# Performance work log

Hardware: AMD Instinct MI355X
Metric: run time of the kernel (lower is better)

## Reference

```python
import jax, jax.numpy as jnp
import numpy as np
import math

B, T, D = 4, 4096, 512
LN_EPS = 1e-5


def setup_inputs() -> dict:
    key = jax.random.key(0)
    ks = jax.random.split(key, 12)
    stdv = 1.0 / math.sqrt(D)
    lin = 1.0 / math.sqrt(D)  # torch Linear default init bound
    return {
        "query": jax.random.normal(ks[0], (B, T, D), jnp.float32),
        "value": jax.random.normal(ks[1], (B, T, D), jnp.float32),
        "query_vector": jax.random.uniform(ks[2], (D,), jnp.float32, -stdv, stdv),
        "key_vector": jax.random.uniform(ks[3], (D,), jnp.float32, -stdv, stdv),
        "value_vector": jax.random.uniform(ks[4], (D,), jnp.float32, -stdv, stdv),
        "Wq": jax.random.uniform(ks[5], (D, D), jnp.float32, -lin, lin),
        "bq": jax.random.uniform(ks[6], (D,), jnp.float32, -lin, lin),
        "ln_gamma": jnp.ones((D,), jnp.float32),
        "ln_beta": jnp.zeros((D,), jnp.float32),
        "Ws": jax.random.uniform(ks[7], (D, D), jnp.float32, -lin, lin),
        "bs": jax.random.uniform(ks[8], (D,), jnp.float32, -lin, lin),
        "Wt": jax.random.uniform(ks[9], (D, D), jnp.float32, -lin, lin),
        "bt": jax.random.uniform(ks[10], (D,), jnp.float32, -lin, lin),
    }


def reference(query, value, query_vector, key_vector, value_vector,
              Wq, bq, ln_gamma, ln_beta, Ws, bs, Wt, bt):
    d = query.shape[-1]
    # query linear + layernorm
    q = query @ Wq.T + bq
    mu = jnp.mean(q, axis=-1, keepdims=True)
    var = jnp.var(q, axis=-1, keepdims=True)
    q = (q - mu) * jax.lax.rsqrt(var + LN_EPS) * ln_gamma + ln_beta
    # gated Q/K/V preprocessing
    q = q * jax.nn.sigmoid(query_vector)
    k = value * jax.nn.sigmoid(key_vector)
    vv = jax.nn.sigmoid(value_vector)              # [D]
    v_sigm = jax.nn.sigmoid(vv @ Ws.T + bs)        # [D] (infer=False path)
    v_tanh = jnp.tanh(vv @ Wt.T + bt)              # [D]
    v = value * (v_sigm * v_tanh)
    # causal full attention (explicit, as in original)
    w = jnp.einsum('btd,bsd->bts', q, k) / jnp.sqrt(jnp.float32(d))
    tmask = jnp.tril(jnp.ones((q.shape[1], q.shape[1]), bool))
    w = jnp.where(tmask[None, :, :], w, -jnp.inf)
    w = jax.nn.softmax(w, axis=-1)
    return jnp.einsum('bts,bsd->btd', w, v)
```

## Files before the change

kernel.cpp:

```cpp
#include <hip/hip_runtime.h>
#include <cstdint>

typedef __bf16 bf16x8 __attribute__((ext_vector_type(8)));
typedef float f32x4 __attribute__((ext_vector_type(4)));

#define DIM 512
#define TSEQ 4096

__device__ __forceinline__ ushort f2bf(float x) {
  uint32_t u = __float_as_uint(x);
  u += 0x7fffu + ((u >> 16) & 1u);
  return (ushort)(u >> 16);
}
__device__ __forceinline__ float bf2f(ushort u) {
  return __uint_as_float(((uint32_t)u) << 16);
}

__global__ __launch_bounds__(512)
void gates_kernel(const float* __restrict__ qv, const float* __restrict__ kv,
                  const float* __restrict__ vvec,
                  const float* __restrict__ Ws, const float* __restrict__ bs,
                  const float* __restrict__ Wt, const float* __restrict__ bt,
                  const float* __restrict__ gamma, const float* __restrict__ beta,
                  float* __restrict__ gk, float* __restrict__ gv,
                  float* __restrict__ gb1, float* __restrict__ gb2) {
  __shared__ float vv[DIM];
  const int t = threadIdx.x;
  const int lane = t & 63, w = t >> 6;
  vv[t] = 1.f / (1.f + __expf(-vvec[t]));
  if (blockIdx.x == 0) {
    const float SC = 0.044194173824159216f;
    float gqv = 1.f / (1.f + __expf(-qv[t]));
    gk[t] = 1.f / (1.f + __expf(-kv[t]));
    gb1[t] = gamma[t] * gqv * SC;
    gb2[t] = beta[t] * gqv * SC;
  }
  __syncthreads();
  const int d = blockIdx.x * 8 + w;
  const float* wsr = Ws + (size_t)d * DIM + lane * 8;
  const float* wtr = Wt + (size_t)d * DIM + lane * 8;
  float4 v0 = *(const float4*)(&vv[lane * 8]);
  float4 v1 = *(const float4*)(&vv[lane * 8 + 4]);
  float4 s0 = *(const float4*)wsr, s1 = *(const float4*)(wsr + 4);
  float4 t0 = *(const float4*)wtr, t1 = *(const float4*)(wtr + 4);
  float as = v0.x*s0.x + v0.y*s0.y + v0.z*s0.z + v0.w*s0.w
           + v1.x*s1.x + v1.y*s1.y + v1.z*s1.z + v1.w*s1.w;
  float at = v0.x*t0.x + v0.y*t0.y + v0.z*t0.z + v0.w*t0.w
           + v1.x*t1.x + v1.y*t1.y + v1.z*t1.z + v1.w*t1.w;
  #pragma unroll
  for (int off = 1; off < 64; off <<= 1) {
    as += __shfl_xor(as, off, 64);
    at += __shfl_xor(at, off, 64);
  }
  if (lane == 0) {
    float sg = 1.f / (1.f + __expf(-(as + bs[d])));
    float th = tanhf(at + bt[d]);
    gv[d] = sg * th;
  }
}

__global__ __launch_bounds__(256)
void wconv_kernel(const float* __restrict__ W, ushort* __restrict__ Wb) {
  int i = blockIdx.x * 256 + threadIdx.x;
  float4 v = ((const float4*)W)[i];
  ushort4 o = { f2bf(v.x), f2bf(v.y), f2bf(v.z), f2bf(v.w) };
  ((ushort4*)Wb)[i] = o;
}

__global__ __launch_bounds__(256, 2)
void qgemmln_kernel(const float* __restrict__ A, const ushort* __restrict__ Wb,
                    const float* __restrict__ bq,
                    const float* __restrict__ gb1, const float* __restrict__ gb2,
                    ushort* __restrict__ qout) {
  __shared__ ushort As[32][40];
  __shared__ float rws[4][32], rws2[4][32];
  const int t = threadIdx.x;
  const int lane = t & 63, w = t >> 6;
  const int r16 = lane & 15, kb8 = lane >> 4;
  const int rowbase = blockIdx.x * 32;
  f32x4 acc[2][8];
  #pragma unroll
  for (int m = 0; m < 2; ++m)
    #pragma unroll
    for (int n = 0; n < 8; ++n) acc[m][n] = (f32x4)0.f;

  for (int kb = 0; kb < 16; ++kb) {
    const int k0 = kb * 32;
    __syncthreads();
    {
      int ar = t >> 3, ac = (t & 7) * 4;
      float4 a = *(const float4*)(A + (size_t)(rowbase + ar) * DIM + k0 + ac);
      ushort4 u = { f2bf(a.x), f2bf(a.y), f2bf(a.z), f2bf(a.w) };
      *(ushort4*)&As[ar][ac] = u;
    }
    __syncthreads();
    bf16x8 a0 = *(const bf16x8*)&As[r16][kb8 * 8];
    bf16x8 a1 = *(const bf16x8*)&As[16 + r16][kb8 * 8];
    #pragma unroll
    for (int n = 0; n < 8; ++n) {
      bf16x8 bb = *(const bf16x8*)(Wb + (size_t)(w * 128 + n * 16 + r16) * DIM + k0 + kb8 * 8);
      acc[0][n] = __builtin_amdgcn_mfma_f32_16x16x32_bf16(a0, bb, acc[0][n], 0, 0, 0);
      acc[1][n] = __builtin_amdgcn_mfma_f32_16x16x32_bf16(a1, bb, acc[1][n], 0, 0, 0);
    }
  }
  float s_[2][4], ss_[2][4];
  #pragma unroll
  for (int m = 0; m < 2; ++m)
    #pragma unroll
    for (int r = 0; r < 4; ++r) { s_[m][r] = 0.f; ss_[m][r] = 0.f; }
  #pragma unroll
  for (int n = 0; n < 8; ++n) {
    float bqv = bq[w * 128 + n * 16 + r16];
    #pragma unroll
    for (int m = 0; m < 2; ++m)
      #pragma unroll
      for (int r = 0; r < 4; ++r) {
        float v = acc[m][n][r] + bqv;
        acc[m][n][r] = v;
        s_[m][r] += v;
        ss_[m][r] += v * v;
      }
  }
  #pragma unroll
  for (int m = 0; m < 2; ++m)
    #pragma unroll
    for (int r = 0; r < 4; ++r)
      #pragma unroll
      for (int off = 1; off < 16; off <<= 1) {
        s_[m][r]  += __shfl_xor(s_[m][r], off, 64);
        ss_[m][r] += __shfl_xor(ss_[m][r], off, 64);
      }
  if (r16 == 0) {
    #pragma unroll
    for (int m = 0; m < 2; ++m)
      #pragma unroll
      for (int r = 0; r < 4; ++r) {
        int row = m * 16 + kb8 * 4 + r;
        rws[w][row]  = s_[m][r];
        rws2[w][row] = ss_[m][r];
      }
  }
  __syncthreads();
  float mu_[2][4], rs_[2][4];
  #pragma unroll
  for (int m = 0; m < 2; ++m)
    #pragma unroll
    for (int r = 0; r < 4; ++r) {
      int row = m * 16 + kb8 * 4 + r;
      float s = rws[0][row] + rws[1][row] + rws[2][row] + rws[3][row];
      float q = rws2[0][row] + rws2[1][row] + rws2[2][row] + rws2[3][row];
      float mu = s * (1.f / DIM);
      float var = q * (1.f / DIM) - mu * mu;
      mu_[m][r] = mu;
      rs_[m][r] = rsqrtf(var + 1e-5f);
    }
  #pragma unroll
  for (int n = 0; n < 8; ++n) {
    int col = w * 128 + n * 16 + r16;
    float g1 = gb1[col], g2 = gb2[col];
    #pragma unroll
    for (int m = 0; m < 2; ++m)
      #pragma unroll
      for (int r = 0; r < 4; ++r) {
        int row = rowbase + m * 16 + kb8 * 4 + r;
        float o = (acc[m][n][r] - mu_[m][r]) * rs_[m][r] * g1 + g2;
        qout[(size_t)row * DIM + col] = f2bf(o);
      }
  }
}

__global__ __launch_bounds__(256)
void vkprep_kernel(const float* __restrict__ value, const float* __restrict__ gk,
                   const float* __restrict__ gv,
                   ushort* __restrict__ kbuf, ushort* __restrict__ vT) {
  __shared__ ushort tile[64][73];
  const int t = threadIdx.x;
  const int s0 = blockIdx.x * 64, d0 = blockIdx.y * 64;
  const size_t boff = (size_t)blockIdx.z * TSEQ * DIM;
  #pragma unroll
  for (int rep = 0; rep < 4; ++rep) {
    int f = rep * 1024 + t * 4;
    int sr = f >> 6, dc = f & 63;
    float4 v = *(const float4*)(value + boff + (size_t)(s0 + sr) * DIM + d0 + dc);
    float4 g = *(const float4*)(gv + d0 + dc);
    float4 gg = *(const float4*)(gk + d0 + dc);
    tile[sr][dc]     = f2bf(v.x * g.x);
    tile[sr][dc + 1] = f2bf(v.y * g.y);
    tile[sr][dc + 2] = f2bf(v.z * g.z);
    tile[sr][dc + 3] = f2bf(v.w * g.w);
    ushort4 ko = { f2bf(v.x*gg.x), f2bf(v.y*gg.y), f2bf(v.z*gg.z), f2bf(v.w*gg.w) };
    *(ushort4*)(kbuf + boff + (size_t)(s0 + sr) * DIM + d0 + dc) = ko;
  }
  __syncthreads();
  const int d = t >> 2, sc0 = (t & 3) * 16;
  __align__(16) ushort tmp[16];
  #pragma unroll
  for (int j = 0; j < 16; ++j) tmp[j] = tile[sc0 + j][d];
  ushort* dst = vT + (size_t)blockIdx.z * DIM * TSEQ + (size_t)(d0 + d) * TSEQ + s0 + sc0;
  ((uint4*)dst)[0] = *(const uint4*)&tmp[0];
  ((uint4*)dst)[1] = *(const uint4*)&tmp[8];
}

__global__ __launch_bounds__(512)
void attn6_kernel(const ushort* __restrict__ qb, const ushort* __restrict__ kb,
                  const ushort* __restrict__ vT, float* __restrict__ out,
                  ushort* __restrict__ pO, float* __restrict__ stats) {
  __shared__ __align__(16) float Sp[4][64][68];
  __shared__ __align__(16) ushort P[64][72];
  __shared__ float lrow[64];

  const int t = threadIdx.x;
  const int lane = t & 63;
  const int w = t >> 6;
  const int r16 = lane & 15;
  const int kb8 = lane >> 4;
  const int dcQ = w & 3;
  const int h = w >> 2;

  const int bid = blockIdx.x;
  const int wg = ((bid & 7) << 5) | (bid >> 3);
  const int b = wg >> 6;
  const int rr = wg & 63;
  const int s = rr >> 1;
  const int half = rr & 1;

  const size_t boff  = (size_t)b * TSEQ * DIM;
  const size_t vboff = (size_t)b * DIM * TSEQ;

  for (int ji = 0; ji < 2; ++ji) {
    int qt, kt0, kt1, mode, cid;
    if (half) {
      if (ji) break;
      qt = 63 - s; kt0 = 31 - s; kt1 = 64 - s; mode = 1; cid = (b*32 + s)*2 + 1;
    } else if (ji == 0) {
      qt = s; kt0 = 0; kt1 = s + 1; mode = 0; cid = 0;
    } else {
      qt = 63 - s; kt0 = 0; kt1 = 31 - s; mode = 1; cid = (b*32 + s)*2;
    }
    const int qbase = qt * 64;

    __syncthreads();
    if (t < 64) lrow[t] = 0.f;
    bf16x8 aQ[4][4];
    #pragma unroll
    for (int m = 0; m < 4; ++m)
      #pragma unroll
      for (int c = 0; c < 4; ++c)
        aQ[m][c] = *(const bf16x8*)(qb + boff + (size_t)(qbase + m*16 + r16) * DIM
                                    + dcQ*128 + c*32 + kb8*8);
    f32x4 accO[4][4];
    #pragma unroll
    for (int m = 0; m < 4; ++m)
      #pragma unroll
      for (int n = 0; n < 4; ++n) accO[m][n] = (f32x4)0.f;

    {
      const int kbase = kt0 * 64;
      f32x4 accS[4][2];
      #pragma unroll
      for (int m = 0; m < 4; ++m) { accS[m][0] = (f32x4)0.f; accS[m][1] = (f32x4)0.f; }
      #pragma unroll
      for (int c = 0; c < 4; ++c) {
        bf16x8 bK0 = *(const bf16x8*)(kb + boff + (size_t)(kbase + h*32 + r16) * DIM
                                      + dcQ*128 + c*32 + kb8*8);
        bf16x8 bK1 = *(const bf16x8*)(kb + boff + (size_t)(kbase + h*32 + 16 + r16) * DIM
                                      + dcQ*128 + c*32 + kb8*8);
        #pragma unroll
        for (int m = 0; m < 4; ++m) {
          accS[m][0] = __builtin_amdgcn_mfma_f32_16x16x32_bf16(bK0, aQ[m][c], accS[m][0], 0, 0, 0);
          accS[m][1] = __builtin_amdgcn_mfma_f32_16x16x32_bf16(bK1, aQ[m][c], accS[m][1], 0, 0, 0);
        }
      }
      #pragma unroll
      for (int m = 0; m < 4; ++m)
        #pragma unroll
        for (int n = 0; n < 2; ++n)
          *(f32x4*)&Sp[dcQ][m*16 + r16][h*32 + n*16 + kb8*4] = accS[m][n];
    }
    __syncthreads();

    for (int kt = kt0; kt < kt1; ++kt) {
      const int kbase = kt * 64;
      const bool havek = (kt + 1 < kt1);

      bf16x8 kpre[8], vpre[8];
      if (havek) {
        const int kb2 = (kt + 1) * 64;
        #pragma unroll
        for (int c = 0; c < 4; ++c) {
          kpre[c*2]     = *(const bf16x8*)(kb + boff + (size_t)(kb2 + h*32 + r16) * DIM
                                           + dcQ*128 + c*32 + kb8*8);
          kpre[c*2 + 1] = *(const bf16x8*)(kb + boff + (size_t)(kb2 + h*32 + 16 + r16) * DIM
                                           + dcQ*128 + c*32 + kb8*8);
        }
      }
      #pragma unroll
      for (int n = 0; n < 4; ++n)
        #pragma unroll
        for (int c = 0; c < 2; ++c)
          vpre[n*2 + c] = *(const bf16x8*)(vT + vboff + (size_t)(w*64 + n*16 + r16) * TSEQ
                                           + kbase + c*32 + kb8*8);

      {
        const int row = t >> 3, c0 = (t & 7) * 8;
        float sv[8];
        #pragma unroll
        for (int j = 0; j < 8; ++j) sv[j] = 0.f;
        #pragma unroll
        for (int ch = 0; ch < 4; ++ch) {
          float4 u0 = *(const float4*)&Sp[ch][row][c0];
          float4 u1 = *(const float4*)&Sp[ch][row][c0 + 4];
          sv[0] += u0.x; sv[1] += u0.y; sv[2] += u0.z; sv[3] += u0.w;
          sv[4] += u1.x; sv[5] += u1.y; sv[6] += u1.z; sv[7] += u1.w;
        }
        const int qg = qbase + row;
        float ps = 0.f;
        #pragma unroll
        for (int j = 0; j < 8; ++j) {
          sv[j] = (kbase + c0 + j > qg) ? 0.f : __expf(sv[j]);
          ps += sv[j];
        }
        ps += __shfl_xor(ps, 1, 64);
        ps += __shfl_xor(ps, 2, 64);
        ps += __shfl_xor(ps, 4, 64);
        ushort4 p0 = { f2bf(sv[0]), f2bf(sv[1]), f2bf(sv[2]), f2bf(sv[3]) };
        ushort4 p1 = { f2bf(sv[4]), f2bf(sv[5]), f2bf(sv[6]), f2bf(sv[7]) };
        *(ushort4*)&P[row][c0] = p0;
        *(ushort4*)&P[row][c0 + 4] = p1;
        if ((t & 7) == 0) lrow[row] += ps;
      }
      __syncthreads();

      __builtin_amdgcn_s_setprio(1);
      #pragma unroll
      for (int c = 0; c < 2; ++c) {
        bf16x8 aP[4];
        #pragma unroll
        for (int m = 0; m < 4; ++m) aP[m] = *(const bf16x8*)&P[m*16 + r16][c*32 + kb8*8];
        #pragma unroll
        for (int n = 0; n < 4; ++n)
          #pragma unroll
          for (int m = 0; m < 4; ++m)
            accO[m][n] = __builtin_amdgcn_mfma_f32_16x16x32_bf16(aP[m], vpre[n*2 + c],
                                                                 accO[m][n], 0, 0, 0);
      }
      if (havek) {
        f32x4 accS[4][2];
        #pragma unroll
        for (int m = 0; m < 4; ++m) { accS[m][0] = (f32x4)0.f; accS[m][1] = (f32x4)0.f; }
        #pragma unroll
        for (int c = 0; c < 4; ++c)
          #pragma unroll
          for (int m = 0; m < 4; ++m) {
            accS[m][0] = __builtin_amdgcn_mfma_f32_16x16x32_bf16(kpre[c*2],     aQ[m][c], accS[m][0], 0, 0, 0);
            accS[m][1] = __builtin_amdgcn_mfma_f32_16x16x32_bf16(kpre[c*2 + 1], aQ[m][c], accS[m][1], 0, 0, 0);
          }
        #pragma unroll
        for (int m = 0; m < 4; ++m)
          #pragma unroll
          for (int n = 0; n < 2; ++n)
            *(f32x4*)&Sp[dcQ][m*16 + r16][h*32 + n*16 + kb8*4] = accS[m][n];
      }
      __builtin_amdgcn_s_setprio(0);
      __syncthreads();
    }

    if (mode == 0) {
      #pragma unroll
      for (int m = 0; m < 4; ++m)
        #pragma unroll
        for (int r = 0; r < 4; ++r) {
          int row = m*16 + kb8*4 + r;
          float inv = 1.f / lrow[row];
          float* dst = out + boff + (size_t)(qbase + row) * DIM + w*64 + r16;
          #pragma unroll
          for (int n = 0; n < 4; ++n) dst[n*16] = accO[m][n][r] * inv;
        }
    } else {
      ushort* po = pO + (size_t)cid * (64 * DIM);
      #pragma unroll
      for (int m = 0; m < 4; ++m)
        #pragma unroll
        for (int r = 0; r < 4; ++r) {
          int row = m*16 + kb8*4 + r;
          ushort* dst = po + (size_t)row * DIM + w*64 + r16;
          #pragma unroll
          for (int n = 0; n < 4; ++n) dst[n*16] = f2bf(accO[m][n][r]);
        }
      if (t < 64) stats[(size_t)cid*64 + t] = lrow[t];
    }
  }
}

__global__ __launch_bounds__(256)
void comb_kernel(const ushort* __restrict__ pO, const float* __restrict__ stats,
                 float* __restrict__ out) {
  const int g = blockIdx.x;
  const int rb = blockIdx.y;
  const int t = threadIdx.x;
  const int b = g >> 5, s = g & 31, qt = 63 - s;
  const int row = rb * 4 + (t >> 6);
  const int col = (t & 63) * 8;
  float l0 = stats[(size_t)(g*2 + 0)*64 + row];
  float l1 = stats[(size_t)(g*2 + 1)*64 + row];
  float inv = 1.f / (l0 + l1);
  const ushort* pa = pO + ((size_t)(g*2 + 0) * 64 + row) * DIM + col;
  const ushort* pb = pO + ((size_t)(g*2 + 1) * 64 + row) * DIM + col;
  ushort4 a0 = ((const ushort4*)pa)[0], a1 = ((const ushort4*)pa)[1];
  ushort4 b0 = ((const ushort4*)pb)[0], b1 = ((const ushort4*)pb)[1];
  float* dst = out + ((size_t)b * TSEQ + (size_t)qt * 64 + row) * DIM + col;
  float4 o0 = { (bf2f(a0.x) + bf2f(b0.x)) * inv, (bf2f(a0.y) + bf2f(b0.y)) * inv,
                (bf2f(a0.z) + bf2f(b0.z)) * inv, (bf2f(a0.w) + bf2f(b0.w)) * inv };
  float4 o1 = { (bf2f(a1.x) + bf2f(b1.x)) * inv, (bf2f(a1.y) + bf2f(b1.y)) * inv,
                (bf2f(a1.z) + bf2f(b1.z)) * inv, (bf2f(a1.w) + bf2f(b1.w)) * inv };
  ((float4*)dst)[0] = o0;
  ((float4*)dst)[1] = o1;
}

extern "C" void kernel_launch(void* const* d_in, const int* in_sizes, int n_in,
                              void* d_out, int out_size, void* d_ws, size_t ws_size,
                              hipStream_t stream) {
  const float* query = (const float*)d_in[0];
  const float* value = (const float*)d_in[1];
  const float* qv    = (const float*)d_in[2];
  const float* kv    = (const float*)d_in[3];
  const float* vvec  = (const float*)d_in[4];
  const float* Wq    = (const float*)d_in[5];
  const float* bq    = (const float*)d_in[6];
  const float* gam   = (const float*)d_in[7];
  const float* bet   = (const float*)d_in[8];
  const float* Ws    = (const float*)d_in[9];
  const float* bs    = (const float*)d_in[10];
  const float* Wt    = (const float*)d_in[11];
  const float* bt    = (const float*)d_in[12];
  float* out = (float*)d_out;

  char* ws = (char*)d_ws;
  float*  gk    = (float*)(ws);
  float*  gv    = (float*)(ws + 2048);
  float*  gb1   = (float*)(ws + 4096);
  float*  gb2   = (float*)(ws + 6144);
  ushort* Wb    = (ushort*)(ws + 8192);
  float*  stats = (float*)(ws + 532480);
  ushort* pO    = (ushort*)(ws + 663552);
  ushort* qb    = (ushort*)(ws + 17440768);
  ushort* kb    = (ushort*)(ws + 34217984);
  ushort* vT    = (ushort*)(ws + 50995200);

  gates_kernel<<<64, 512, 0, stream>>>(qv, kv, vvec, Ws, bs, Wt, bt, gam, bet,
                                       gk, gv, gb1, gb2);
  wconv_kernel<<<256, 256, 0, stream>>>(Wq, Wb);
  qgemmln_kernel<<<512, 256, 0, stream>>>(query, Wb, bq, gb1, gb2, qb);
  vkprep_kernel<<<dim3(64, 8, 4), 256, 0, stream>>>(value, gk, gv, kb, vT);
  attn6_kernel<<<256, 512, 0, stream>>>(qb, kb, vT, out, pO, stats);
  comb_kernel<<<dim3(128, 16), 256, 0, stream>>>(pO, stats, out);
}
```

Before: 224.4 us.

## Stage K and V tiles in LDS via direct global-to-LDS loads, repartition waves

The attention kernel now copies each 64-row K tile and each V^T tile into swizzled LDS buffers with global_load_lds DMA, instead of having each wave load its own register fragments from global memory. Waves are repartitioned so each computes full-depth QK^T for 16 query rows and half the key columns. This removes the four partial score buffers and their cross-wave reduction, and each wave covers 32 query rows by 128 output columns in PV. LDS use grows to about 155 KB, which allows only one block per CU. The V load is no longer overlapped with the softmax, and correctness depends on the async LDS writes being complete before the barriers.

```diff
diff --git a/kernel.cpp b/kernel.cpp
--- a/kernel.cpp
+++ b/kernel.cpp
@@ -14,6 +14,12 @@
 }
 __device__ __forceinline__ float bf2f(ushort u) {
   return __uint_as_float(((uint32_t)u) << 16);
+}
+
+typedef __attribute__((address_space(3))) uint32_t lds_u32;
+typedef __attribute__((address_space(1))) const uint32_t glb_u32;
+__device__ __forceinline__ void gload16(const ushort* g, ushort* l) {
+  __builtin_amdgcn_global_load_lds((glb_u32*)g, (lds_u32*)l, 16, 0, 0);
 }
 
 __global__ __launch_bounds__(512)
@@ -202,10 +208,12 @@
 }
 
 __global__ __launch_bounds__(512)
-void attn6_kernel(const ushort* __restrict__ qb, const ushort* __restrict__ kb,
+void attn9_kernel(const ushort* __restrict__ qb, const ushort* __restrict__ kb,
                   const ushort* __restrict__ vT, float* __restrict__ out,
                   ushort* __restrict__ pO, float* __restrict__ stats) {
-  __shared__ __align__(16) float Sp[4][64][68];
+  __shared__ __align__(16) ushort Kl[64 * 512];
+  __shared__ __align__(16) ushort Vl[512 * 64];
+  __shared__ __align__(16) float Sp[64][68];
   __shared__ __align__(16) ushort P[64][72];
   __shared__ float lrow[64];
 
@@ -214,8 +222,10 @@
   const int w = t >> 6;
   const int r16 = lane & 15;
   const int kb8 = lane >> 4;
-  const int dcQ = w & 3;
-  const int h = w >> 2;
+  const int sq = w >> 1;
+  const int kh = w & 1;
+  const int qh = w >> 2;
+  const int dcol = (w & 3) * 128;
 
   const int bid = blockIdx.x;
   const int wg = ((bid & 7) << 5) | (bid >> 3);
@@ -226,6 +236,12 @@
 
   const size_t boff  = (size_t)b * TSEQ * DIM;
   const size_t vboff = (size_t)b * DIM * TSEQ;
+
+  const int kst_row = w;
+  const int kst_src = ((lane ^ w) & 63) * 8;
+  const int vst_d   = t >> 3;
+  const int vst_src = (((t & 7) ^ ((t >> 3) & 7))) * 8;
+  const int vst_g   = (t & 7) * 8;
 
   for (int ji = 0; ji < 2; ++ji) {
     int qt, kt0, kt1, mode, cid;
@@ -241,41 +257,41 @@
 
     __syncthreads();
     if (t < 64) lrow[t] = 0.f;
-    bf16x8 aQ[4][4];
-    #pragma unroll
-    for (int m = 0; m < 4; ++m)
-      #pragma unroll
-      for (int c = 0; c < 4; ++c)
-        aQ[m][c] = *(const bf16x8*)(qb + boff + (size_t)(qbase + m*16 + r16) * DIM
-                                    + dcQ*128 + c*32 + kb8*8);
-    f32x4 accO[4][4];
-    #pragma unroll
-    for (int m = 0; m < 4; ++m)
-      #pragma unroll
-      for (int n = 0; n < 4; ++n) accO[m][n] = (f32x4)0.f;
+
+    bf16x8 aQ[16];
+    #pragma unroll
+    for (int c = 0; c < 16; ++c)
+      aQ[c] = *(const bf16x8*)(qb + boff + (size_t)(qbase + sq*16 + r16) * DIM
+                               + c*32 + kb8*8);
+    f32x4 accO[2][8];
+    #pragma unroll
+    for (int m = 0; m < 2; ++m)
+      #pragma unroll
+      for (int n = 0; n < 8; ++n) accO[m][n] = (f32x4)0.f;
 
     {
-      const int kbase = kt0 * 64;
-      f32x4 accS[4][2];
-      #pragma unroll
-      for (int m = 0; m < 4; ++m) { accS[m][0] = (f32x4)0.f; accS[m][1] = (f32x4)0.f; }
-      #pragma unroll
-      for (int c = 0; c < 4; ++c) {
-        bf16x8 bK0 = *(const bf16x8*)(kb + boff + (size_t)(kbase + h*32 + r16) * DIM
-                                      + dcQ*128 + c*32 + kb8*8);
-        bf16x8 bK1 = *(const bf16x8*)(kb + boff + (size_t)(kbase + h*32 + 16 + r16) * DIM
-                                      + dcQ*128 + c*32 + kb8*8);
-        #pragma unroll
-        for (int m = 0; m < 4; ++m) {
-          accS[m][0] = __builtin_amdgcn_mfma_f32_16x16x32_bf16(bK0, aQ[m][c], accS[m][0], 0, 0, 0);
-          accS[m][1] = __builtin_amdgcn_mfma_f32_16x16x32_bf16(bK1, aQ[m][c], accS[m][1], 0, 0, 0);
-        }
-      }
-      #pragma unroll
-      for (int m = 0; m < 4; ++m)
-        #pragma unroll
-        for (int n = 0; n < 2; ++n)
-          *(f32x4*)&Sp[dcQ][m*16 + r16][h*32 + n*16 + kb8*4] = accS[m][n];
+      const ushort* kbp = kb + boff + (size_t)(kt0 * 64) * DIM;
+      #pragma unroll
+      for (int rd = 0; rd < 8; ++rd)
+        gload16(kbp + (size_t)(rd*8 + kst_row) * DIM + kst_src,
+                Kl + (rd*8 + kst_row) * DIM + lane * 8);
+    }
+    __syncthreads();
+    {
+      f32x4 accS[2];
+      accS[0] = (f32x4)0.f; accS[1] = (f32x4)0.f;
+      #pragma unroll
+      for (int c = 0; c < 16; ++c) {
+        #pragma unroll
+        for (int n = 0; n < 2; ++n) {
+          int krow = kh*32 + n*16 + r16;
+          bf16x8 kf = *(const bf16x8*)(Kl + krow*DIM + (((c*4 + kb8) ^ (r16 & 7)))*8);
+          accS[n] = __builtin_amdgcn_mfma_f32_16x16x32_bf16(kf, aQ[c], accS[n], 0, 0, 0);
+        }
+      }
+      #pragma unroll
+      for (int n = 0; n < 2; ++n)
+        *(f32x4*)&Sp[sq*16 + r16][kh*32 + n*16 + kb8*4] = accS[n];
     }
     __syncthreads();
 
@@ -283,36 +299,25 @@
       const int kbase = kt * 64;
       const bool havek = (kt + 1 < kt1);
 
-      bf16x8 kpre[8], vpre[8];
+      {
+        const ushort* vp = vT + vboff + kbase;
+        #pragma unroll
+        for (int rd = 0; rd < 8; ++rd)
+          gload16(vp + (size_t)(rd*64 + vst_d) * TSEQ + vst_src,
+                  Vl + (rd*64 + vst_d) * 64 + vst_g);
+      }
       if (havek) {
-        const int kb2 = (kt + 1) * 64;
-        #pragma unroll
-        for (int c = 0; c < 4; ++c) {
-          kpre[c*2]     = *(const bf16x8*)(kb + boff + (size_t)(kb2 + h*32 + r16) * DIM
-                                           + dcQ*128 + c*32 + kb8*8);
-          kpre[c*2 + 1] = *(const bf16x8*)(kb + boff + (size_t)(kb2 + h*32 + 16 + r16) * DIM
-                                           + dcQ*128 + c*32 + kb8*8);
-        }
-      }
-      #pragma unroll
-      for (int n = 0; n < 4; ++n)
-        #pragma unroll
-        for (int c = 0; c < 2; ++c)
-          vpre[n*2 + c] = *(const bf16x8*)(vT + vboff + (size_t)(w*64 + n*16 + r16) * TSEQ
-                                           + kbase + c*32 + kb8*8);
-
+        const ushort* kbp = kb + boff + (size_t)(kbase + 64) * DIM;
+        #pragma unroll
+        for (int rd = 0; rd < 8; ++rd)
+          gload16(kbp + (size_t)(rd*8 + kst_row) * DIM + kst_src,
+                  Kl + (rd*8 + kst_row) * DIM + lane * 8);
+      }
       {
         const int row = t >> 3, c0 = (t & 7) * 8;
-        float sv[8];
-        #pragma unroll
-        for (int j = 0; j < 8; ++j) sv[j] = 0.f;
-        #pragma unroll
-        for (int ch = 0; ch < 4; ++ch) {
-          float4 u0 = *(const float4*)&Sp[ch][row][c0];
-          float4 u1 = *(const float4*)&Sp[ch][row][c0 + 4];
-          sv[0] += u0.x; sv[1] += u0.y; sv[2] += u0.z; sv[3] += u0.w;
-          sv[4] += u1.x; sv[5] += u1.y; sv[6] += u1.z; sv[7] += u1.w;
-        }
+        float4 u0 = *(const float4*)&Sp[row][c0];
+        float4 u1 = *(const float4*)&Sp[row][c0 + 4];
+        float sv[8] = { u0.x, u0.y, u0.z, u0.w, u1.x, u1.y, u1.z, u1.w };
         const int qg = qbase + row;
         float ps = 0.f;
         #pragma unroll
@@ -334,32 +339,31 @@
       __builtin_amdgcn_s_setprio(1);
       #pragma unroll
       for (int c = 0; c < 2; ++c) {
-        bf16x8 aP[4];
-        #pragma unroll
-        for (int m = 0; m < 4; ++m) aP[m] = *(const bf16x8*)&P[m*16 + r16][c*32 + kb8*8];
-        #pragma unroll
-        for (int n = 0; n < 4; ++n)
+        bf16x8 aP0 = *(const bf16x8*)&P[qh*32 + r16][c*32 + kb8*8];
+        bf16x8 aP1 = *(const bf16x8*)&P[qh*32 + 16 + r16][c*32 + kb8*8];
+        #pragma unroll
+        for (int n = 0; n < 8; ++n) {
+          int d = dcol + n*16 + r16;
+          bf16x8 bV = *(const bf16x8*)(Vl + d*64 + (((c*4 + kb8) ^ (r16 & 7)))*8);
+          accO[0][n] = __builtin_amdgcn_mfma_f32_16x16x32_bf16(aP0, bV, accO[0][n], 0, 0, 0);
+          accO[1][n] = __builtin_amdgcn_mfma_f32_16x16x32_bf16(aP1, bV, accO[1][n], 0, 0, 0);
+        }
+      }
+      if (havek) {
+        f32x4 accS[2];
+        accS[0] = (f32x4)0.f; accS[1] = (f32x4)0.f;
+        #pragma unroll
+        for (int c = 0; c < 16; ++c) {
           #pragma unroll
-          for (int m = 0; m < 4; ++m)
-            accO[m][n] = __builtin_amdgcn_mfma_f32_16x16x32_bf16(aP[m], vpre[n*2 + c],
-                                                                 accO[m][n], 0, 0, 0);
-      }
-      if (havek) {
-        f32x4 accS[4][2];
-        #pragma unroll
-        for (int m = 0; m < 4; ++m) { accS[m][0] = (f32x4)0.f; accS[m][1] = (f32x4)0.f; }
-        #pragma unroll
-        for (int c = 0; c < 4; ++c)
-          #pragma unroll
-          for (int m = 0; m < 4; ++m) {
-            accS[m][0] = __builtin_amdgcn_mfma_f32_16x16x32_bf16(kpre[c*2],     aQ[m][c], accS[m][0], 0, 0, 0);
-            accS[m][1] = __builtin_amdgcn_mfma_f32_16x16x32_bf16(kpre[c*2 + 1], aQ[m][c], accS[m][1], 0, 0, 0);
+          for (int n = 0; n < 2; ++n) {
+            int krow = kh*32 + n*16 + r16;
+            bf16x8 kf = *(const bf16x8*)(Kl + krow*DIM + (((c*4 + kb8) ^ (r16 & 7)))*8);
+            accS[n] = __builtin_amdgcn_mfma_f32_16x16x32_bf16(kf, aQ[c], accS[n], 0, 0, 0);
           }
-        #pragma unroll
-        for (int m = 0; m < 4; ++m)
-          #pragma unroll
-          for (int n = 0; n < 2; ++n)
-            *(f32x4*)&Sp[dcQ][m*16 + r16][h*32 + n*16 + kb8*4] = accS[m][n];
+        }
+        #pragma unroll
+        for (int n = 0; n < 2; ++n)
+          *(f32x4*)&Sp[sq*16 + r16][kh*32 + n*16 + kb8*4] = accS[n];
       }
       __builtin_amdgcn_s_setprio(0);
       __syncthreads();
@@ -367,25 +371,25 @@
 
     if (mode == 0) {
       #pragma unroll
-      for (int m = 0; m < 4; ++m)
+      for (int m = 0; m < 2; ++m)
         #pragma unroll
         for (int r = 0; r < 4; ++r) {
-          int row = m*16 + kb8*4 + r;
+          int row = qh*32 + m*16 + kb8*4 + r;
           float inv = 1.f / lrow[row];
-          float* dst = out + boff + (size_t)(qbase + row) * DIM + w*64 + r16;
+          float* dst = out + boff + (size_t)(qbase + row) * DIM + dcol + r16;
           #pragma unroll
-          for (int n = 0; n < 4; ++n) dst[n*16] = accO[m][n][r] * inv;
+          for (int n = 0; n < 8; ++n) dst[n*16] = accO[m][n][r] * inv;
         }
     } else {
       ushort* po = pO + (size_t)cid * (64 * DIM);
       #pragma unroll
-      for (int m = 0; m < 4; ++m)
+      for (int m = 0; m < 2; ++m)
         #pragma unroll
         for (int r = 0; r < 4; ++r) {
-          int row = m*16 + kb8*4 + r;
-          ushort* dst = po + (size_t)row * DIM + w*64 + r16;
+          int row = qh*32 + m*16 + kb8*4 + r;
+          ushort* dst = po + (size_t)row * DIM + dcol + r16;
           #pragma unroll
-          for (int n = 0; n < 4; ++n) dst[n*16] = f2bf(accO[m][n][r]);
+          for (int n = 0; n < 8; ++n) dst[n*16] = f2bf(accO[m][n][r]);
         }
       if (t < 64) stats[(size_t)cid*64 + t] = lrow[t];
     }
@@ -452,6 +456,6 @@
   wconv_kernel<<<256, 256, 0, stream>>>(Wq, Wb);
   qgemmln_kernel<<<512, 256, 0, stream>>>(query, Wb, bq, gb1, gb2, qb);
   vkprep_kernel<<<dim3(64, 8, 4), 256, 0, stream>>>(value, gk, gv, kb, vT);
-  attn6_kernel<<<256, 512, 0, stream>>>(qb, kb, vT, out, pO, stats);
+  attn9_kernel<<<256, 512, 0, stream>>>(qb, kb, vT, out, pO, stats);
   comb_kernel<<<dim3(128, 16), 256, 0, stream>>>(pO, stats, out);
 }
```

New measurement: 181.0 us. 19.3% less time.
